# Optimization experiments

Measured on AMD Instinct MI355X. Metric: run time of the kernel, lower is better.

## Reference

```python
import jax, jax.numpy as jnp
import numpy as np

B, S, D_IN, D_OUT = 4, 2048, 2048, 2048


def setup_inputs() -> dict:
    key = jax.random.key(0)
    k1, k2, k3, k4 = jax.random.split(key, 4)
    x = jax.random.normal(k1, (B, S, D_IN), dtype=jnp.float32)
    scale = 1.0 / np.sqrt(D_IN)
    Wq = jax.random.normal(k2, (D_IN, D_OUT), dtype=jnp.float32) * scale
    Wk = jax.random.normal(k3, (D_IN, D_OUT), dtype=jnp.float32) * scale
    Wv = jax.random.normal(k4, (D_IN, D_OUT), dtype=jnp.float32) * scale
    return {"x": x, "Wq": Wq, "Wk": Wk, "Wv": Wv}


def reference(x, Wq, Wk, Wv):
    # x: [B,S,D_in]; Wq/Wk/Wv: [D_in,D_out]
    q = x @ Wq  # [B,S,D_out]
    k = x @ Wk
    v = x @ Wv
    d_out = q.shape[-1]
    inv_sqrt_d = jnp.asarray(1.0 / np.sqrt(d_out), dtype=x.dtype)
    scores = jnp.einsum('bqd,bkd->bqk', q, k) * inv_sqrt_d  # [B,S,S]
    n = scores.shape[-1]
    causal = jnp.tril(jnp.ones((n, n), dtype=bool))  # True where attending allowed
    scores = jnp.where(causal[None, :, :], scores, jnp.asarray(-jnp.inf, scores.dtype))
    attn = jax.nn.softmax(scores, axis=-1)  # dropout p=0.0 -> identity
    return jnp.einsum('bqk,bkd->bqd', attn, v)  # [B,S,D_out]
```

## Files before the change

kernel.cpp:

```cpp
#include <hip/hip_runtime.h>
#include <cmath>

typedef __bf16 bfx8 __attribute__((ext_vector_type(8)));
typedef float f32x4 __attribute__((ext_vector_type(4)));
typedef unsigned short u16x8 __attribute__((ext_vector_type(8)));

static constexpr int BB = 4, SS = 2048, DD = 2048;

__device__ __forceinline__ unsigned short f2bf(float f) {
  unsigned u = __builtin_bit_cast(unsigned, f);
  u += 0x7fffu + ((u >> 16) & 1u);
  return (unsigned short)(u >> 16);
}

__device__ __forceinline__ void gload_lds16(const void* g, void* l) {
  __builtin_amdgcn_global_load_lds(
      (__attribute__((address_space(1))) unsigned int*)(g),
      (__attribute__((address_space(3))) unsigned int*)(l),
      16, 0, 0);
}

template <int CMODE>
__global__ __launch_bounds__(512, 2) void gemm_bt(
    const unsigned short* __restrict__ A, const unsigned short* __restrict__ B,
    void* __restrict__ Cv, int N, int K,
    long long sA, long long sB, long long sC, float scale)
{
  const int bx = blockIdx.x, by = blockIdx.y, bz = blockIdx.z;
  if (CMODE == 1 && bx > by) return;
  const int t = threadIdx.x;
  const int wave = t >> 6, lane = t & 63;
  const int fr = lane & 15, fk = lane >> 4;
  const int wr = wave >> 2;
  const int wc = wave & 3;
  const int m0 = by << 8, n0 = bx << 8;

  __shared__ __align__(16) char lds[131072];

  const unsigned short* Ab = A + (size_t)bz * sA;
  const unsigned short* Bb = B + (size_t)bz * sB;

  const unsigned short* aS[4];
  const unsigned short* bS[4];
  int lOff[4];
#pragma unroll
  for (int j = 0; j < 4; ++j) {
    int c = ((j >> 1) << 10) + ((j & 1) << 9) + t;
    int row = c >> 3;
    int sb = ((c & 7) << 4) ^ ((row & 7) << 4);
    aS[j] = Ab + (size_t)(m0 + row) * K + (sb >> 1);
    bS[j] = Bb + (size_t)(n0 + row) * K + (sb >> 1);
    lOff[j] = ((j >> 1) << 14) + ((j & 1) << 13) + (wave << 10);
  }

  int ktiles = K >> 6;
  if (CMODE == 2) ktiles = min(ktiles, (by + 1) * 4);

  f32x4 acc[8][4] = {};
  const int sx = (fr & 7) << 4;
  const int aRowB = wr << 7;
  const int bRowB = wc << 6;

#pragma unroll
  for (int j = 0; j < 4; ++j) { gload_lds16(aS[j], lds + lOff[j]); aS[j] += 64; }
#pragma unroll
  for (int j = 0; j < 4; ++j) { gload_lds16(bS[j], lds + 32768 + lOff[j]); bS[j] += 64; }
  asm volatile("s_waitcnt vmcnt(0)" ::: "memory");
  __builtin_amdgcn_s_barrier();

  for (int kt = 0; kt < ktiles; ++kt) {
    const int cb = (kt & 1) << 16;
    const int nb = cb ^ 65536;
    const bool pf = (kt + 1 < ktiles);
    const char* la = lds + cb;
    const char* lb = lds + cb + 32768;
#pragma unroll
    for (int q = 0; q < 4; ++q) {
      const int mb = (q & 1) << 2;
      const int nbf = (q >> 1) << 1;
      bfx8 af[4][2], bv[2][2];
#pragma unroll
      for (int mi = 0; mi < 4; ++mi) {
        int row = aRowB + ((mb + mi) << 4) + fr;
#pragma unroll
        for (int kk = 0; kk < 2; ++kk)
          af[mi][kk] = *(const bfx8*)(la + row * 128 + (((kk << 6) + (fk << 4)) ^ sx));
      }
#pragma unroll
      for (int ni = 0; ni < 2; ++ni) {
        int row = bRowB + ((nbf + ni) << 4) + fr;
#pragma unroll
        for (int kk = 0; kk < 2; ++kk)
          bv[ni][kk] = *(const bfx8*)(lb + row * 128 + (((kk << 6) + (fk << 4)) ^ sx));
      }
      if (q == 0 && pf) {
#pragma unroll
        for (int j = 0; j < 4; ++j) { gload_lds16(aS[j], lds + nb + lOff[j]); aS[j] += 64; }
      }
      if (q == 1 && pf) {
#pragma unroll
        for (int j = 0; j < 4; ++j) { gload_lds16(bS[j], lds + nb + 32768 + lOff[j]); bS[j] += 64; }
      }
      __builtin_amdgcn_s_barrier();
      asm volatile("s_waitcnt lgkmcnt(0)" ::: "memory");
      __builtin_amdgcn_sched_barrier(0);
      __builtin_amdgcn_s_setprio(1);
#pragma unroll
      for (int kk = 0; kk < 2; ++kk)
#pragma unroll
        for (int mi = 0; mi < 4; ++mi)
#pragma unroll
          for (int ni = 0; ni < 2; ++ni)
            acc[mb + mi][nbf + ni] = __builtin_amdgcn_mfma_f32_16x16x32_bf16(
                af[mi][kk], bv[ni][kk], acc[mb + mi][nbf + ni], 0, 0, 0);
      __builtin_amdgcn_s_setprio(0);
      if (q == 3) asm volatile("s_waitcnt vmcnt(0)" ::: "memory");
      __builtin_amdgcn_s_barrier();
    }
  }

#pragma unroll
  for (int mf = 0; mf < 8; ++mf) {
#pragma unroll
    for (int nf = 0; nf < 4; ++nf) {
      int r0 = m0 + (wr << 7) + (mf << 4) + (fk << 2);
      int cn = n0 + (wc << 6) + (nf << 4) + fr;
      if (CMODE == 0) {
        unsigned short* C = (unsigned short*)Cv + (size_t)bz * sC;
#pragma unroll
        for (int j = 0; j < 4; ++j)
          C[(size_t)(r0 + j) * N + cn] = f2bf(acc[mf][nf][j]);
      } else {
        float* C = (float*)Cv + (size_t)bz * sC;
#pragma unroll
        for (int j = 0; j < 4; ++j)
          C[(size_t)(r0 + j) * N + cn] = acc[mf][nf][j] * scale;
      }
    }
  }
}

__global__ __launch_bounds__(256) void cvt_x_kernel(
    const float* __restrict__ x, unsigned short* __restrict__ xb)
{
  size_t i = ((size_t)blockIdx.x * 256 + threadIdx.x) * 8;
  float4 a = *(const float4*)(x + i);
  float4 b = *(const float4*)(x + i + 4);
  u16x8 o = {f2bf(a.x), f2bf(a.y), f2bf(a.z), f2bf(a.w),
             f2bf(b.x), f2bf(b.y), f2bf(b.z), f2bf(b.w)};
  *(u16x8*)(xb + i) = o;
}

__global__ __launch_bounds__(256) void cvt_wT_kernel(
    const float* __restrict__ Wq, const float* __restrict__ Wk,
    const float* __restrict__ Wv, unsigned short* __restrict__ Wt)
{
  const float* W = blockIdx.z == 0 ? Wq : (blockIdx.z == 1 ? Wk : Wv);
  unsigned short* out = Wt + (size_t)blockIdx.z * DD * DD;
  __shared__ unsigned short tile[64][65];
  int k0 = blockIdx.y * 64, n0 = blockIdx.x * 64;
#pragma unroll
  for (int i = 0; i < 16; ++i) {
    int idx = threadIdx.x + i * 256;
    int r = idx >> 6, c = idx & 63;
    tile[r][c] = f2bf(W[(size_t)(k0 + r) * DD + n0 + c]);
  }
  __syncthreads();
#pragma unroll
  for (int i = 0; i < 16; ++i) {
    int idx = threadIdx.x + i * 256;
    int r = idx >> 6, c = idx & 63;
    out[(size_t)(n0 + r) * DD + k0 + c] = tile[c][r];
  }
}

__global__ __launch_bounds__(256) void softmax_causal(
    const float* __restrict__ Sc, unsigned short* __restrict__ P)
{
  const int i = blockIdx.x, b = blockIdx.y, t = threadIdx.x;
  const float* srow = Sc + ((size_t)b * SS + i) * SS;
  unsigned short* prow = P + ((size_t)b * SS + i) * SS;
  const int j0 = t * 8;
  float4 v0 = *(const float4*)(srow + j0);
  float4 v1 = *(const float4*)(srow + j0 + 4);
  float s[8] = {v0.x, v0.y, v0.z, v0.w, v1.x, v1.y, v1.z, v1.w};
  float mx = -INFINITY;
#pragma unroll
  for (int e = 0; e < 8; ++e) {
    if (j0 + e > i) s[e] = -INFINITY;
    mx = fmaxf(mx, s[e]);
  }
#pragma unroll
  for (int off = 32; off; off >>= 1) mx = fmaxf(mx, __shfl_xor(mx, off));
  __shared__ float red[8];
  if ((t & 63) == 0) red[t >> 6] = mx;
  __syncthreads();
  mx = fmaxf(fmaxf(red[0], red[1]), fmaxf(red[2], red[3]));
  float e8[8];
  float sm = 0.f;
#pragma unroll
  for (int e = 0; e < 8; ++e) {
    e8[e] = (j0 + e <= i) ? __expf(s[e] - mx) : 0.f;
    sm += e8[e];
  }
#pragma unroll
  for (int off = 32; off; off >>= 1) sm += __shfl_xor(sm, off);
  if ((t & 63) == 0) red[4 + (t >> 6)] = sm;
  __syncthreads();
  float inv = 1.0f / (red[4] + red[5] + red[6] + red[7]);
  u16x8 o;
#pragma unroll
  for (int e = 0; e < 8; ++e) o[e] = f2bf(e8[e] * inv);
  *(u16x8*)(prow + j0) = o;
}

extern "C" void kernel_launch(void* const* d_in, const int* in_sizes, int n_in,
                              void* d_out, int out_size, void* d_ws, size_t ws_size,
                              hipStream_t stream)
{
  const float* x  = (const float*)d_in[0];
  const float* Wq = (const float*)d_in[1];
  const float* Wk = (const float*)d_in[2];
  const float* Wv = (const float*)d_in[3];
  float* out = (float*)d_out;

  const size_t MR = (size_t)BB * SS;
  unsigned short* xb = (unsigned short*)d_ws;
  unsigned short* Wt = xb + MR * DD;
  unsigned short* qk = Wt + 3ull * DD * DD;
  unsigned short* vt = qk + 2ull * MR * DD;
  float* sc = (float*)(vt + (size_t)BB * DD * SS);
  unsigned short* P = (unsigned short*)(sc + (size_t)BB * SS * SS);

  cvt_x_kernel<<<dim3(8192), 256, 0, stream>>>(x, xb);
  cvt_wT_kernel<<<dim3(32, 32, 3), 256, 0, stream>>>(Wq, Wk, Wv, Wt);

  gemm_bt<0><<<dim3(8, 32, 2), 512, 0, stream>>>(
      xb, Wt, qk, DD, DD, 0, (long long)DD * DD, (long long)(MR * DD), 1.f);
  gemm_bt<0><<<dim3(8, 8, 4), 512, 0, stream>>>(
      Wt + 2ull * DD * DD, xb, vt, SS, DD,
      0, (long long)(SS * (size_t)DD), (long long)(DD * (size_t)SS), 1.f);

  const float iscale = 1.0f / sqrtf((float)DD);
  gemm_bt<1><<<dim3(8, 8, 4), 512, 0, stream>>>(
      qk, qk + MR * DD, sc, SS, DD,
      (long long)(SS * (size_t)DD), (long long)(SS * (size_t)DD),
      (long long)(SS * (size_t)SS), iscale);

  softmax_causal<<<dim3(SS, BB), 256, 0, stream>>>(sc, P);

  gemm_bt<2><<<dim3(8, 8, 4), 512, 0, stream>>>(
      P, vt, out, DD, SS,
      (long long)(SS * (size_t)SS), (long long)(DD * (size_t)SS),
      (long long)(SS * (size_t)DD), 1.f);
}
```

Before: 506.9 us.

## Restructure GEMM k-loop into single-barrier stage and add block-order swizzle

Replaces the four-quadrant inner loop, which had two barriers per quadrant, with a single pass per k-tile. All prefetches for the next tile are issued up front, the B fragments are loaded once, A fragments are streamed per row-block into MFMAs, and there is one wait and barrier at the end. It also remaps the block index so that consecutive blocks walk down columns, aiming for better L2 reuse. The goal is less barrier and synchronisation overhead and fewer duplicate LDS fragment reads. The cost is less interleaving of LDS reads with MFMAs, and the swizzle hardcodes a grid x of 8.

```diff
diff --git a/kernel.cpp b/kernel.cpp
--- a/kernel.cpp
+++ b/kernel.cpp
@@ -26,7 +26,9 @@
     void* __restrict__ Cv, int N, int K,
     long long sA, long long sB, long long sC, float scale)
 {
-  const int bx = blockIdx.x, by = blockIdx.y, bz = blockIdx.z;
+  const int lid = (blockIdx.y << 3) | blockIdx.x;
+  const int swz = (lid & 7) * gridDim.y + (lid >> 3);
+  const int bx = swz & 7, by = swz >> 3, bz = blockIdx.z;
   if (CMODE == 1 && bx > by) return;
   const int t = threadIdx.x;
   const int wave = t >> 6, lane = t & 63;
@@ -71,52 +73,41 @@
   for (int kt = 0; kt < ktiles; ++kt) {
     const int cb = (kt & 1) << 16;
     const int nb = cb ^ 65536;
-    const bool pf = (kt + 1 < ktiles);
     const char* la = lds + cb;
-    const char* lb = lds + cb + 32768;
-#pragma unroll
-    for (int q = 0; q < 4; ++q) {
-      const int mb = (q & 1) << 2;
-      const int nbf = (q >> 1) << 1;
-      bfx8 af[4][2], bv[2][2];
-#pragma unroll
-      for (int mi = 0; mi < 4; ++mi) {
-        int row = aRowB + ((mb + mi) << 4) + fr;
-#pragma unroll
-        for (int kk = 0; kk < 2; ++kk)
-          af[mi][kk] = *(const bfx8*)(la + row * 128 + (((kk << 6) + (fk << 4)) ^ sx));
-      }
-#pragma unroll
-      for (int ni = 0; ni < 2; ++ni) {
-        int row = bRowB + ((nbf + ni) << 4) + fr;
-#pragma unroll
-        for (int kk = 0; kk < 2; ++kk)
-          bv[ni][kk] = *(const bfx8*)(lb + row * 128 + (((kk << 6) + (fk << 4)) ^ sx));
-      }
-      if (q == 0 && pf) {
-#pragma unroll
-        for (int j = 0; j < 4; ++j) { gload_lds16(aS[j], lds + nb + lOff[j]); aS[j] += 64; }
-      }
-      if (q == 1 && pf) {
-#pragma unroll
-        for (int j = 0; j < 4; ++j) { gload_lds16(bS[j], lds + nb + 32768 + lOff[j]); bS[j] += 64; }
-      }
-      __builtin_amdgcn_s_barrier();
-      asm volatile("s_waitcnt lgkmcnt(0)" ::: "memory");
-      __builtin_amdgcn_sched_barrier(0);
-      __builtin_amdgcn_s_setprio(1);
+    const char* lb = la + 32768;
+
+    if (kt + 1 < ktiles) {
+#pragma unroll
+      for (int j = 0; j < 4; ++j) { gload_lds16(aS[j], lds + nb + lOff[j]); aS[j] += 64; }
+#pragma unroll
+      for (int j = 0; j < 4; ++j) { gload_lds16(bS[j], lds + nb + 32768 + lOff[j]); bS[j] += 64; }
+    }
+
+    bfx8 bv[4][2];
+#pragma unroll
+    for (int ni = 0; ni < 4; ++ni) {
+      int row = bRowB + (ni << 4) + fr;
 #pragma unroll
       for (int kk = 0; kk < 2; ++kk)
-#pragma unroll
-        for (int mi = 0; mi < 4; ++mi)
-#pragma unroll
-          for (int ni = 0; ni < 2; ++ni)
-            acc[mb + mi][nbf + ni] = __builtin_amdgcn_mfma_f32_16x16x32_bf16(
-                af[mi][kk], bv[ni][kk], acc[mb + mi][nbf + ni], 0, 0, 0);
-      __builtin_amdgcn_s_setprio(0);
-      if (q == 3) asm volatile("s_waitcnt vmcnt(0)" ::: "memory");
-      __builtin_amdgcn_s_barrier();
-    }
+        bv[ni][kk] = *(const bfx8*)(lb + row * 128 + ((((kk << 6) | (fk << 4))) ^ sx));
+    }
+    __builtin_amdgcn_s_setprio(1);
+#pragma unroll
+    for (int mi = 0; mi < 8; ++mi) {
+      int row = aRowB + (mi << 4) + fr;
+      bfx8 a0 = *(const bfx8*)(la + row * 128 + (((fk << 4)) ^ sx));
+      bfx8 a1 = *(const bfx8*)(la + row * 128 + ((64 | (fk << 4)) ^ sx));
+#pragma unroll
+      for (int ni = 0; ni < 4; ++ni)
+        acc[mi][ni] = __builtin_amdgcn_mfma_f32_16x16x32_bf16(a0, bv[ni][0], acc[mi][ni], 0, 0, 0);
+#pragma unroll
+      for (int ni = 0; ni < 4; ++ni)
+        acc[mi][ni] = __builtin_amdgcn_mfma_f32_16x16x32_bf16(a1, bv[ni][1], acc[mi][ni], 0, 0, 0);
+    }
+    __builtin_amdgcn_s_setprio(0);
+
+    asm volatile("s_waitcnt vmcnt(0) lgkmcnt(0)" ::: "memory");
+    __builtin_amdgcn_s_barrier();
   }
 
 #pragma unroll
```

New measurement: 472.0 us. 1.07x faster.
